# Kernel optimization log

Measured on AMD Instinct MI355X. Metric: run time of the kernel, lower is better.

The kernel has to match this reference:

```python
import jax, jax.numpy as jnp
import numpy as np

HEADS = 8
WH, WW = 8, 8
DIM = 256
B = 4096
N = WH * WW  # 64


def _rel_index():
    ch, cw = np.meshgrid(np.arange(WH), np.arange(WW), indexing='ij')
    coords = np.stack([ch.ravel(), cw.ravel()])  # (2, N)
    rel = coords[:, :, None] - coords[:, None, :]  # (2, N, N)
    rel = rel.transpose(1, 2, 0)
    rel[:, :, 0] += WH - 1
    rel[:, :, 1] += WW - 1
    rel[:, :, 0] *= 2 * WW - 1
    return jnp.asarray(rel.sum(-1), dtype=jnp.int32)  # (N, N)


def setup_inputs() -> dict:
    key = jax.random.key(0)
    ks = jax.random.split(key, 6)
    x = jax.random.normal(ks[0], (B, N, DIM), dtype=jnp.float32)
    attn_mask = jnp.zeros((1, HEADS, N, N), dtype=jnp.float32)
    w_qkv = jax.random.normal(ks[1], (3 * DIM, DIM), dtype=jnp.float32) * 0.02
    w_proj = jax.random.normal(ks[2], (DIM, DIM), dtype=jnp.float32) * 0.02
    b_proj = jax.random.normal(ks[3], (DIM,), dtype=jnp.float32) * 0.02
    table = jax.random.normal(ks[4], (225, HEADS), dtype=jnp.float32) * 0.02
    return {"x": x, "attn_mask": attn_mask, "w_qkv": w_qkv, "w_proj": w_proj,
            "b_proj": b_proj, "table": table, "rel_index": _rel_index()}


def reference(x, attn_mask, w_qkv, w_proj, b_proj, table, rel_index):
    Bn, Nn, C = x.shape
    hd = C // HEADS
    qkv = (x @ w_qkv.T).reshape(Bn, Nn, 3, HEADS, hd)
    q = qkv[:, :, 0].transpose(0, 2, 1, 3)  # (B,h,N,d)
    k = qkv[:, :, 1].transpose(0, 2, 1, 3)
    v = qkv[:, :, 2].transpose(0, 2, 1, 3)
    scale = 1.0 / jnp.sqrt(jnp.asarray(hd, dtype=x.dtype))
    attn = jnp.einsum('bhnd,bhmd->bhnm', q, k) * scale
    bias = table[rel_index]  # (N,N,h)
    attn = attn + bias.transpose(2, 0, 1)[None] + attn_mask
    attn = jax.nn.softmax(attn, axis=-1)
    out = jnp.einsum('bhnm,bhmd->bhnd', attn, v)
    out = out.transpose(0, 2, 1, 3).reshape(Bn, Nn, C)
    return out @ w_proj.T + b_proj
```

## Files before the change

kernel.cpp:

```cpp
#include <hip/hip_runtime.h>
#include <hip/hip_bf16.h>

#define HEADS 8
#define NTOK 64
#define DIM 256

typedef __attribute__((ext_vector_type(8))) short bf16x8;
typedef __attribute__((ext_vector_type(4))) short bf16x4;
typedef __attribute__((ext_vector_type(4))) float f32x4;
typedef unsigned short u16;

__device__ __forceinline__ u16 nf2bf(float f) {
    __hip_bfloat16 b = __float2bfloat16(f);
    return *reinterpret_cast<u16*>(&b);
}

__global__ void prep_kernel(const float* __restrict__ wqkv,
                            const float* __restrict__ wproj,
                            const float* __restrict__ table,
                            const int* __restrict__ rel_index,
                            const float* __restrict__ mask,
                            u16* __restrict__ wq_bf,
                            u16* __restrict__ wp_bf,
                            float* __restrict__ bias) {
    const int NQ = 768 * 256;
    const int NP = 256 * 256;
    const int NB = HEADS * NTOK * NTOK;
    int total = NQ + NP + NB;
    for (int i = blockIdx.x * blockDim.x + threadIdx.x; i < total;
         i += gridDim.x * blockDim.x) {
        if (i < NQ) {
            wq_bf[i] = nf2bf(wqkv[i]);
        } else if (i < NQ + NP) {
            wp_bf[i - NQ] = nf2bf(wproj[i - NQ]);
        } else {
            int j = i - (NQ + NP);
            int h = j >> 12;
            int nm = j & 4095;
            bias[j] = (table[rel_index[nm] * HEADS + h] + mask[j])
                      * 1.4426950408889634f;
        }
    }
}

__launch_bounds__(512, 2)
__global__ void win_attn_kernel(const float* __restrict__ x,
                                const u16* __restrict__ wq_bf,
                                const u16* __restrict__ wp_bf,
                                const float* __restrict__ bias,
                                const float* __restrict__ b_proj,
                                float* __restrict__ out) {
    __shared__ u16 smem[33792];
    u16* s_x = smem;
    u16* s_o = smem + 16896;

    const int b = blockIdx.x;
    const int tid = threadIdx.x;
    const int w = tid >> 6;
    const int l = tid & 63;
    const int l16 = l & 15;
    const int lhi = l >> 4;
    const int h = w;

    const u16* rq0 = wq_bf + (h * 32 + l16) * 256;
    const u16* rq1 = rq0 + 16 * 256;
    const u16* rk0 = wq_bf + (256 + h * 32 + l16) * 256;
    const u16* rk1 = rk0 + 16 * 256;
    const u16* rv0 = wq_bf + (512 + h * 32 + l16) * 256;
    const u16* rv1 = rv0 + 16 * 256;

    bf16x8 aq0 = *reinterpret_cast<const bf16x8*>(rq0 + lhi * 8);
    bf16x8 aq1 = *reinterpret_cast<const bf16x8*>(rq1 + lhi * 8);
    bf16x8 ak0 = *reinterpret_cast<const bf16x8*>(rk0 + lhi * 8);
    bf16x8 ak1 = *reinterpret_cast<const bf16x8*>(rk1 + lhi * 8);
    bf16x8 av0 = *reinterpret_cast<const bf16x8*>(rv0 + lhi * 8);
    bf16x8 av1 = *reinterpret_cast<const bf16x8*>(rv1 + lhi * 8);
    bf16x8 bq0 = *reinterpret_cast<const bf16x8*>(rq0 + 32 + lhi * 8);
    bf16x8 bq1 = *reinterpret_cast<const bf16x8*>(rq1 + 32 + lhi * 8);
    bf16x8 bk0 = *reinterpret_cast<const bf16x8*>(rk0 + 32 + lhi * 8);
    bf16x8 bk1 = *reinterpret_cast<const bf16x8*>(rk1 + 32 + lhi * 8);
    bf16x8 bv0 = *reinterpret_cast<const bf16x8*>(rv0 + 32 + lhi * 8);
    bf16x8 bv1 = *reinterpret_cast<const bf16x8*>(rv1 + 32 + lhi * 8);

    const float* xw = x + (size_t)b * (NTOK * DIM);
#pragma unroll
    for (int it = 0; it < 8; ++it) {
        int idx4 = tid + it * 512;
        float4 v = reinterpret_cast<const float4*>(xw)[idx4];
        int row = idx4 >> 6;
        int col = (idx4 & 63) * 4;
        ushort4 o;
        o.x = nf2bf(v.x); o.y = nf2bf(v.y); o.z = nf2bf(v.z); o.w = nf2bf(v.w);
        *reinterpret_cast<ushort4*>(&s_x[row * 264 + col]) = o;
    }
    __syncthreads();

    f32x4 qacc[2][4], kacc[2][4], vacc[4][2];
    const f32x4 zero = {0.f, 0.f, 0.f, 0.f};
#pragma unroll
    for (int ct = 0; ct < 2; ++ct)
#pragma unroll
        for (int tt = 0; tt < 4; ++tt) {
            qacc[ct][tt] = zero; kacc[ct][tt] = zero; vacc[tt][ct] = zero;
        }

    for (int ks = 0; ks < 8; ++ks) {
        const int k0 = ks * 32 + lhi * 8;
        bf16x8 xf[4];
#pragma unroll
        for (int tt = 0; tt < 4; ++tt)
            xf[tt] = *reinterpret_cast<const bf16x8*>(&s_x[(tt * 16 + l16) * 264 + k0]);
        bf16x8 nq0, nq1, nk0, nk1, nv0, nv1;
        if (ks < 6) {
            nq0 = *reinterpret_cast<const bf16x8*>(rq0 + k0 + 64);
            nq1 = *reinterpret_cast<const bf16x8*>(rq1 + k0 + 64);
            nk0 = *reinterpret_cast<const bf16x8*>(rk0 + k0 + 64);
            nk1 = *reinterpret_cast<const bf16x8*>(rk1 + k0 + 64);
            nv0 = *reinterpret_cast<const bf16x8*>(rv0 + k0 + 64);
            nv1 = *reinterpret_cast<const bf16x8*>(rv1 + k0 + 64);
        }
#pragma unroll
        for (int tt = 0; tt < 4; ++tt) {
            qacc[0][tt] = __builtin_amdgcn_mfma_f32_16x16x32_bf16(aq0, xf[tt], qacc[0][tt], 0, 0, 0);
            qacc[1][tt] = __builtin_amdgcn_mfma_f32_16x16x32_bf16(aq1, xf[tt], qacc[1][tt], 0, 0, 0);
            kacc[0][tt] = __builtin_amdgcn_mfma_f32_16x16x32_bf16(ak0, xf[tt], kacc[0][tt], 0, 0, 0);
            kacc[1][tt] = __builtin_amdgcn_mfma_f32_16x16x32_bf16(ak1, xf[tt], kacc[1][tt], 0, 0, 0);
            vacc[tt][0] = __builtin_amdgcn_mfma_f32_16x16x32_bf16(xf[tt], av0, vacc[tt][0], 0, 0, 0);
            vacc[tt][1] = __builtin_amdgcn_mfma_f32_16x16x32_bf16(xf[tt], av1, vacc[tt][1], 0, 0, 0);
        }
        aq0 = bq0; aq1 = bq1; ak0 = bk0; ak1 = bk1; av0 = bv0; av1 = bv1;
        bq0 = nq0; bq1 = nq1; bk0 = nk0; bk1 = nk1; bv0 = nv0; bv1 = nv1;
    }

    bf16x4 qf[4][2], kf[4][2], vf[4][2];
#pragma unroll
    for (int tt = 0; tt < 4; ++tt)
#pragma unroll
        for (int ct = 0; ct < 2; ++ct) {
            bf16x4 q, k, v;
#pragma unroll
            for (int r = 0; r < 4; ++r) {
                q[r] = (short)nf2bf(qacc[ct][tt][r]);
                k[r] = (short)nf2bf(kacc[ct][tt][r]);
                v[r] = (short)nf2bf(vacc[tt][ct][r]);
            }
            qf[tt][ct] = q; kf[tt][ct] = k; vf[tt][ct] = v;
        }

    {
        const float scale = 0.17677669529663687f * 1.4426950408889634f;
        const float* biash = bias + h * 4096;
        f32x4 bias_c[4], bias_n[4];
#pragma unroll
        for (int mt = 0; mt < 4; ++mt)
            bias_c[mt] = *reinterpret_cast<const f32x4*>(
                &biash[l16 * 64 + mt * 16 + lhi * 4]);

#pragma unroll
        for (int nt = 0; nt < 4; ++nt) {
            if (nt < 3) {
#pragma unroll
                for (int mt = 0; mt < 4; ++mt)
                    bias_n[mt] = *reinterpret_cast<const f32x4*>(
                        &biash[((nt + 1) * 16 + l16) * 64 + mt * 16 + lhi * 4]);
            }
            f32x4 sacc[4];
#pragma unroll
            for (int mt = 0; mt < 4; ++mt) {
                sacc[mt] = __builtin_amdgcn_mfma_f32_16x16x16bf16_1k(kf[mt][0], qf[nt][0], zero, 0, 0, 0);
                sacc[mt] = __builtin_amdgcn_mfma_f32_16x16x16bf16_1k(kf[mt][1], qf[nt][1], sacc[mt], 0, 0, 0);
            }
            float p[4][4];
            float sum = 0.f;
#pragma unroll
            for (int mt = 0; mt < 4; ++mt)
#pragma unroll
                for (int r = 0; r < 4; ++r) {
                    p[mt][r] = exp2f(sacc[mt][r] * scale + bias_c[mt][r]);
                    sum += p[mt][r];
                }
            sum += __shfl_xor(sum, 16, 64);
            sum += __shfl_xor(sum, 32, 64);
            float inv = 1.0f / sum;
            bf16x4 pf[4];
#pragma unroll
            for (int mt = 0; mt < 4; ++mt) {
                bf16x4 pk;
#pragma unroll
                for (int r = 0; r < 4; ++r) pk[r] = (short)nf2bf(p[mt][r]);
                pf[mt] = pk;
            }
            f32x4 oa0 = zero, oa1 = zero;
#pragma unroll
            for (int mt = 0; mt < 4; ++mt) {
                oa0 = __builtin_amdgcn_mfma_f32_16x16x16bf16_1k(vf[mt][0], pf[mt], oa0, 0, 0, 0);
                oa1 = __builtin_amdgcn_mfma_f32_16x16x16bf16_1k(vf[mt][1], pf[mt], oa1, 0, 0, 0);
            }
            {
                ushort4 o0, o1;
                o0.x = nf2bf(oa0[0] * inv); o0.y = nf2bf(oa0[1] * inv);
                o0.z = nf2bf(oa0[2] * inv); o0.w = nf2bf(oa0[3] * inv);
                o1.x = nf2bf(oa1[0] * inv); o1.y = nf2bf(oa1[1] * inv);
                o1.z = nf2bf(oa1[2] * inv); o1.w = nf2bf(oa1[3] * inv);
                u16* orow = &s_o[(nt * 16 + l16) * 264 + h * 32 + lhi * 4];
                *reinterpret_cast<ushort4*>(orow) = o0;
                *reinterpret_cast<ushort4*>(orow + 16) = o1;
            }
            if (nt < 3) {
#pragma unroll
                for (int mt = 0; mt < 4; ++mt) bias_c[mt] = bias_n[mt];
            }
        }
    }
    __syncthreads();

    f32x4 acc3[2][4];
#pragma unroll
    for (int t = 0; t < 2; ++t)
#pragma unroll
        for (int tt = 0; tt < 4; ++tt) acc3[t][tt] = zero;

    const u16* prow0 = wp_bf + (w * 16 + l16) * 256;
    const u16* prow1 = wp_bf + ((w + 8) * 16 + l16) * 256;
    bf16x8 wp0 = *reinterpret_cast<const bf16x8*>(prow0 + lhi * 8);
    bf16x8 wp1 = *reinterpret_cast<const bf16x8*>(prow1 + lhi * 8);
    for (int ks = 0; ks < 8; ++ks) {
        const int k0 = ks * 32 + lhi * 8;
        bf16x8 np0, np1;
        if (ks < 7) {
            np0 = *reinterpret_cast<const bf16x8*>(prow0 + k0 + 32);
            np1 = *reinterpret_cast<const bf16x8*>(prow1 + k0 + 32);
        }
#pragma unroll
        for (int tt = 0; tt < 4; ++tt) {
            bf16x8 of = *reinterpret_cast<const bf16x8*>(&s_o[(tt * 16 + l16) * 264 + k0]);
            acc3[0][tt] = __builtin_amdgcn_mfma_f32_16x16x32_bf16(wp0, of, acc3[0][tt], 0, 0, 0);
            acc3[1][tt] = __builtin_amdgcn_mfma_f32_16x16x32_bf16(wp1, of, acc3[1][tt], 0, 0, 0);
        }
        wp0 = np0; wp1 = np1;
    }
    float* outw = out + (size_t)b * (NTOK * DIM);
#pragma unroll
    for (int t = 0; t < 2; ++t) {
        int colb = (w + t * 8) * 16 + lhi * 4;
        float4 bp = *reinterpret_cast<const float4*>(&b_proj[colb]);
#pragma unroll
        for (int tt = 0; tt < 4; ++tt) {
            float4 o;
            o.x = acc3[t][tt][0] + bp.x;
            o.y = acc3[t][tt][1] + bp.y;
            o.z = acc3[t][tt][2] + bp.z;
            o.w = acc3[t][tt][3] + bp.w;
            *reinterpret_cast<float4*>(&outw[(tt * 16 + l16) * 256 + colb]) = o;
        }
    }
}

extern "C" void kernel_launch(void* const* d_in, const int* in_sizes, int n_in,
                              void* d_out, int out_size, void* d_ws, size_t ws_size,
                              hipStream_t stream) {
    const float* x     = (const float*)d_in[0];
    const float* mask  = (const float*)d_in[1];
    const float* wqkv  = (const float*)d_in[2];
    const float* wproj = (const float*)d_in[3];
    const float* bproj = (const float*)d_in[4];
    const float* table = (const float*)d_in[5];
    const int*   relix = (const int*)d_in[6];

    u16*   wq_bf = (u16*)d_ws;
    u16*   wp_bf = wq_bf + 768 * 256;
    float* bias  = (float*)(wp_bf + 256 * 256);

    prep_kernel<<<64, 512, 0, stream>>>(wqkv, wproj, table, relix, mask,
                                        wq_bf, wp_bf, bias);
    win_attn_kernel<<<4096, 512, 0, stream>>>(x, wq_bf, wp_bf, bias, bproj,
                                              (float*)d_out);
}
```

Measured before the change: 385.1 us.

## Process two windows per block and interleave QKV and projection GEMMs across them

Each block now handles two windows, halving the grid. The x load for the second window is issued before the first window's attention, and the second window's QKV GEMM is fused into one loop with the first window's output projection. The aim is to hide global-load latency and keep the MFMA units busy across stage boundaries. The cost is much higher register pressure from holding q/k/v fragments, accumulators and staged x together at launch bounds (512,2), which could cause spills. Weight loads in the fused loop also lose their software prefetch.

```diff
diff --git a/kernel.cpp b/kernel.cpp
--- a/kernel.cpp
+++ b/kernel.cpp
@@ -51,10 +51,12 @@
                                 const float* __restrict__ b_proj,
                                 float* __restrict__ out) {
     __shared__ u16 smem[33792];
-    u16* s_x = smem;
-    u16* s_o = smem + 16896;
-
-    const int b = blockIdx.x;
+    u16* buf0 = smem;
+    u16* buf1 = smem + 16896;
+
+    const int bid = blockIdx.x;
+    const int winA = bid * 2;
+    const int winB = bid * 2 + 1;
     const int tid = threadIdx.x;
     const int w = tid >> 6;
     const int l = tid & 63;
@@ -68,107 +70,116 @@
     const u16* rk1 = rk0 + 16 * 256;
     const u16* rv0 = wq_bf + (512 + h * 32 + l16) * 256;
     const u16* rv1 = rv0 + 16 * 256;
-
-    bf16x8 aq0 = *reinterpret_cast<const bf16x8*>(rq0 + lhi * 8);
-    bf16x8 aq1 = *reinterpret_cast<const bf16x8*>(rq1 + lhi * 8);
-    bf16x8 ak0 = *reinterpret_cast<const bf16x8*>(rk0 + lhi * 8);
-    bf16x8 ak1 = *reinterpret_cast<const bf16x8*>(rk1 + lhi * 8);
-    bf16x8 av0 = *reinterpret_cast<const bf16x8*>(rv0 + lhi * 8);
-    bf16x8 av1 = *reinterpret_cast<const bf16x8*>(rv1 + lhi * 8);
-    bf16x8 bq0 = *reinterpret_cast<const bf16x8*>(rq0 + 32 + lhi * 8);
-    bf16x8 bq1 = *reinterpret_cast<const bf16x8*>(rq1 + 32 + lhi * 8);
-    bf16x8 bk0 = *reinterpret_cast<const bf16x8*>(rk0 + 32 + lhi * 8);
-    bf16x8 bk1 = *reinterpret_cast<const bf16x8*>(rk1 + 32 + lhi * 8);
-    bf16x8 bv0 = *reinterpret_cast<const bf16x8*>(rv0 + 32 + lhi * 8);
-    bf16x8 bv1 = *reinterpret_cast<const bf16x8*>(rv1 + 32 + lhi * 8);
-
-    const float* xw = x + (size_t)b * (NTOK * DIM);
-#pragma unroll
-    for (int it = 0; it < 8; ++it) {
-        int idx4 = tid + it * 512;
-        float4 v = reinterpret_cast<const float4*>(xw)[idx4];
-        int row = idx4 >> 6;
-        int col = (idx4 & 63) * 4;
-        ushort4 o;
-        o.x = nf2bf(v.x); o.y = nf2bf(v.y); o.z = nf2bf(v.z); o.w = nf2bf(v.w);
-        *reinterpret_cast<ushort4*>(&s_x[row * 264 + col]) = o;
+    const u16* prow0 = wp_bf + (w * 16 + l16) * 256;
+    const u16* prow1 = wp_bf + ((w + 8) * 16 + l16) * 256;
+    const float* biash = bias + h * 4096;
+    const f32x4 zero = {0.f, 0.f, 0.f, 0.f};
+    const float scale = 0.17677669529663687f * 1.4426950408889634f;
+
+    const float4 bp0 = *reinterpret_cast<const float4*>(&b_proj[w * 16 + lhi * 4]);
+    const float4 bp1 = *reinterpret_cast<const float4*>(&b_proj[(w + 8) * 16 + lhi * 4]);
+
+    {
+        const float* xw = x + (size_t)winA * (NTOK * DIM);
+#pragma unroll
+        for (int it = 0; it < 8; ++it) {
+            int idx4 = tid + it * 512;
+            float4 v = reinterpret_cast<const float4*>(xw)[idx4];
+            int row = idx4 >> 6;
+            int col = (idx4 & 63) * 4;
+            ushort4 o;
+            o.x = nf2bf(v.x); o.y = nf2bf(v.y); o.z = nf2bf(v.z); o.w = nf2bf(v.w);
+            *reinterpret_cast<ushort4*>(&buf0[row * 264 + col]) = o;
+        }
     }
     __syncthreads();
 
-    f32x4 qacc[2][4], kacc[2][4], vacc[4][2];
-    const f32x4 zero = {0.f, 0.f, 0.f, 0.f};
-#pragma unroll
-    for (int ct = 0; ct < 2; ++ct)
-#pragma unroll
-        for (int tt = 0; tt < 4; ++tt) {
-            qacc[ct][tt] = zero; kacc[ct][tt] = zero; vacc[tt][ct] = zero;
-        }
-
-    for (int ks = 0; ks < 8; ++ks) {
-        const int k0 = ks * 32 + lhi * 8;
-        bf16x8 xf[4];
+    bf16x4 qfA[4][2], kfA[4][2], vfA[4][2];
+    {
+        f32x4 qacc[2][4], kacc[2][4], vacc[4][2];
+#pragma unroll
+        for (int ct = 0; ct < 2; ++ct)
+#pragma unroll
+            for (int tt = 0; tt < 4; ++tt) {
+                qacc[ct][tt] = zero; kacc[ct][tt] = zero; vacc[tt][ct] = zero;
+            }
+        bf16x8 aq0 = *reinterpret_cast<const bf16x8*>(rq0 + lhi * 8);
+        bf16x8 aq1 = *reinterpret_cast<const bf16x8*>(rq1 + lhi * 8);
+        bf16x8 ak0 = *reinterpret_cast<const bf16x8*>(rk0 + lhi * 8);
+        bf16x8 ak1 = *reinterpret_cast<const bf16x8*>(rk1 + lhi * 8);
+        bf16x8 av0 = *reinterpret_cast<const bf16x8*>(rv0 + lhi * 8);
+        bf16x8 av1 = *reinterpret_cast<const bf16x8*>(rv1 + lhi * 8);
+        bf16x8 bq0 = *reinterpret_cast<const bf16x8*>(rq0 + 32 + lhi * 8);
+        bf16x8 bq1 = *reinterpret_cast<const bf16x8*>(rq1 + 32 + lhi * 8);
+        bf16x8 bk0 = *reinterpret_cast<const bf16x8*>(rk0 + 32 + lhi * 8);
+        bf16x8 bk1 = *reinterpret_cast<const bf16x8*>(rk1 + 32 + lhi * 8);
+        bf16x8 bv0 = *reinterpret_cast<const bf16x8*>(rv0 + 32 + lhi * 8);
+        bf16x8 bv1 = *reinterpret_cast<const bf16x8*>(rv1 + 32 + lhi * 8);
+
+        for (int ks = 0; ks < 8; ++ks) {
+            const int k0 = ks * 32 + lhi * 8;
+            bf16x8 xf[4];
+#pragma unroll
+            for (int tt = 0; tt < 4; ++tt)
+                xf[tt] = *reinterpret_cast<const bf16x8*>(&buf0[(tt * 16 + l16) * 264 + k0]);
+            bf16x8 nq0, nq1, nk0, nk1, nv0, nv1;
+            if (ks < 6) {
+                nq0 = *reinterpret_cast<const bf16x8*>(rq0 + k0 + 64);
+                nq1 = *reinterpret_cast<const bf16x8*>(rq1 + k0 + 64);
+                nk0 = *reinterpret_cast<const bf16x8*>(rk0 + k0 + 64);
+                nk1 = *reinterpret_cast<const bf16x8*>(rk1 + k0 + 64);
+                nv0 = *reinterpret_cast<const bf16x8*>(rv0 + k0 + 64);
+                nv1 = *reinterpret_cast<const bf16x8*>(rv1 + k0 + 64);
+            }
+#pragma unroll
+            for (int tt = 0; tt < 4; ++tt) {
+                qacc[0][tt] = __builtin_amdgcn_mfma_f32_16x16x32_bf16(aq0, xf[tt], qacc[0][tt], 0, 0, 0);
+                qacc[1][tt] = __builtin_amdgcn_mfma_f32_16x16x32_bf16(aq1, xf[tt], qacc[1][tt], 0, 0, 0);
+                kacc[0][tt] = __builtin_amdgcn_mfma_f32_16x16x32_bf16(ak0, xf[tt], kacc[0][tt], 0, 0, 0);
+                kacc[1][tt] = __builtin_amdgcn_mfma_f32_16x16x32_bf16(ak1, xf[tt], kacc[1][tt], 0, 0, 0);
+                vacc[tt][0] = __builtin_amdgcn_mfma_f32_16x16x32_bf16(xf[tt], av0, vacc[tt][0], 0, 0, 0);
+                vacc[tt][1] = __builtin_amdgcn_mfma_f32_16x16x32_bf16(xf[tt], av1, vacc[tt][1], 0, 0, 0);
+            }
+            aq0 = bq0; aq1 = bq1; ak0 = bk0; ak1 = bk1; av0 = bv0; av1 = bv1;
+            bq0 = nq0; bq1 = nq1; bk0 = nk0; bk1 = nk1; bv0 = nv0; bv1 = nv1;
+        }
 #pragma unroll
         for (int tt = 0; tt < 4; ++tt)
-            xf[tt] = *reinterpret_cast<const bf16x8*>(&s_x[(tt * 16 + l16) * 264 + k0]);
-        bf16x8 nq0, nq1, nk0, nk1, nv0, nv1;
-        if (ks < 6) {
-            nq0 = *reinterpret_cast<const bf16x8*>(rq0 + k0 + 64);
-            nq1 = *reinterpret_cast<const bf16x8*>(rq1 + k0 + 64);
-            nk0 = *reinterpret_cast<const bf16x8*>(rk0 + k0 + 64);
-            nk1 = *reinterpret_cast<const bf16x8*>(rk1 + k0 + 64);
-            nv0 = *reinterpret_cast<const bf16x8*>(rv0 + k0 + 64);
-            nv1 = *reinterpret_cast<const bf16x8*>(rv1 + k0 + 64);
-        }
-#pragma unroll
-        for (int tt = 0; tt < 4; ++tt) {
-            qacc[0][tt] = __builtin_amdgcn_mfma_f32_16x16x32_bf16(aq0, xf[tt], qacc[0][tt], 0, 0, 0);
-            qacc[1][tt] = __builtin_amdgcn_mfma_f32_16x16x32_bf16(aq1, xf[tt], qacc[1][tt], 0, 0, 0);
-            kacc[0][tt] = __builtin_amdgcn_mfma_f32_16x16x32_bf16(ak0, xf[tt], kacc[0][tt], 0, 0, 0);
-            kacc[1][tt] = __builtin_amdgcn_mfma_f32_16x16x32_bf16(ak1, xf[tt], kacc[1][tt], 0, 0, 0);
-            vacc[tt][0] = __builtin_amdgcn_mfma_f32_16x16x32_bf16(xf[tt], av0, vacc[tt][0], 0, 0, 0);
-            vacc[tt][1] = __builtin_amdgcn_mfma_f32_16x16x32_bf16(xf[tt], av1, vacc[tt][1], 0, 0, 0);
-        }
-        aq0 = bq0; aq1 = bq1; ak0 = bk0; ak1 = bk1; av0 = bv0; av1 = bv1;
-        bq0 = nq0; bq1 = nq1; bk0 = nk0; bk1 = nk1; bv0 = nv0; bv1 = nv1;
-    }
-
-    bf16x4 qf[4][2], kf[4][2], vf[4][2];
-#pragma unroll
-    for (int tt = 0; tt < 4; ++tt)
-#pragma unroll
-        for (int ct = 0; ct < 2; ++ct) {
-            bf16x4 q, k, v;
-#pragma unroll
-            for (int r = 0; r < 4; ++r) {
-                q[r] = (short)nf2bf(qacc[ct][tt][r]);
-                k[r] = (short)nf2bf(kacc[ct][tt][r]);
-                v[r] = (short)nf2bf(vacc[tt][ct][r]);
-            }
-            qf[tt][ct] = q; kf[tt][ct] = k; vf[tt][ct] = v;
-        }
-
-    {
-        const float scale = 0.17677669529663687f * 1.4426950408889634f;
-        const float* biash = bias + h * 4096;
-        f32x4 bias_c[4], bias_n[4];
-#pragma unroll
-        for (int mt = 0; mt < 4; ++mt)
-            bias_c[mt] = *reinterpret_cast<const f32x4*>(
-                &biash[l16 * 64 + mt * 16 + lhi * 4]);
-
+#pragma unroll
+            for (int ct = 0; ct < 2; ++ct) {
+                bf16x4 q, k, v;
+#pragma unroll
+                for (int r = 0; r < 4; ++r) {
+                    q[r] = (short)nf2bf(qacc[ct][tt][r]);
+                    k[r] = (short)nf2bf(kacc[ct][tt][r]);
+                    v[r] = (short)nf2bf(vacc[tt][ct][r]);
+                }
+                qfA[tt][ct] = q; kfA[tt][ct] = k; vfA[tt][ct] = v;
+            }
+    }
+    __syncthreads();
+
+    float4 xs[8];
+    {
+        const float* xw = x + (size_t)winB * (NTOK * DIM);
+#pragma unroll
+        for (int it = 0; it < 8; ++it)
+            xs[it] = reinterpret_cast<const float4*>(xw)[tid + it * 512];
+    }
+
+    {
+        f32x4 bias_c[4];
 #pragma unroll
         for (int nt = 0; nt < 4; ++nt) {
-            if (nt < 3) {
-#pragma unroll
-                for (int mt = 0; mt < 4; ++mt)
-                    bias_n[mt] = *reinterpret_cast<const f32x4*>(
-                        &biash[((nt + 1) * 16 + l16) * 64 + mt * 16 + lhi * 4]);
-            }
+#pragma unroll
+            for (int mt = 0; mt < 4; ++mt)
+                bias_c[mt] = *reinterpret_cast<const f32x4*>(
+                    &biash[(nt * 16 + l16) * 64 + mt * 16 + lhi * 4]);
             f32x4 sacc[4];
 #pragma unroll
             for (int mt = 0; mt < 4; ++mt) {
-                sacc[mt] = __builtin_amdgcn_mfma_f32_16x16x16bf16_1k(kf[mt][0], qf[nt][0], zero, 0, 0, 0);
-                sacc[mt] = __builtin_amdgcn_mfma_f32_16x16x16bf16_1k(kf[mt][1], qf[nt][1], sacc[mt], 0, 0, 0);
+                sacc[mt] = __builtin_amdgcn_mfma_f32_16x16x16bf16_1k(kfA[mt][0], qfA[nt][0], zero, 0, 0, 0);
+                sacc[mt] = __builtin_amdgcn_mfma_f32_16x16x16bf16_1k(kfA[mt][1], qfA[nt][1], sacc[mt], 0, 0, 0);
             }
             float p[4][4];
             float sum = 0.f;
@@ -193,65 +204,184 @@
             f32x4 oa0 = zero, oa1 = zero;
 #pragma unroll
             for (int mt = 0; mt < 4; ++mt) {
-                oa0 = __builtin_amdgcn_mfma_f32_16x16x16bf16_1k(vf[mt][0], pf[mt], oa0, 0, 0, 0);
-                oa1 = __builtin_amdgcn_mfma_f32_16x16x16bf16_1k(vf[mt][1], pf[mt], oa1, 0, 0, 0);
-            }
-            {
-                ushort4 o0, o1;
-                o0.x = nf2bf(oa0[0] * inv); o0.y = nf2bf(oa0[1] * inv);
-                o0.z = nf2bf(oa0[2] * inv); o0.w = nf2bf(oa0[3] * inv);
-                o1.x = nf2bf(oa1[0] * inv); o1.y = nf2bf(oa1[1] * inv);
-                o1.z = nf2bf(oa1[2] * inv); o1.w = nf2bf(oa1[3] * inv);
-                u16* orow = &s_o[(nt * 16 + l16) * 264 + h * 32 + lhi * 4];
-                *reinterpret_cast<ushort4*>(orow) = o0;
-                *reinterpret_cast<ushort4*>(orow + 16) = o1;
-            }
-            if (nt < 3) {
-#pragma unroll
-                for (int mt = 0; mt < 4; ++mt) bias_c[mt] = bias_n[mt];
-            }
-        }
+                oa0 = __builtin_amdgcn_mfma_f32_16x16x16bf16_1k(vfA[mt][0], pf[mt], oa0, 0, 0, 0);
+                oa1 = __builtin_amdgcn_mfma_f32_16x16x16bf16_1k(vfA[mt][1], pf[mt], oa1, 0, 0, 0);
+            }
+            ushort4 o0, o1;
+            o0.x = nf2bf(oa0[0] * inv); o0.y = nf2bf(oa0[1] * inv);
+            o0.z = nf2bf(oa0[2] * inv); o0.w = nf2bf(oa0[3] * inv);
+            o1.x = nf2bf(oa1[0] * inv); o1.y = nf2bf(oa1[1] * inv);
+            o1.z = nf2bf(oa1[2] * inv); o1.w = nf2bf(oa1[3] * inv);
+            u16* orow = &buf0[(nt * 16 + l16) * 264 + h * 32 + lhi * 4];
+            *reinterpret_cast<ushort4*>(orow) = o0;
+            *reinterpret_cast<ushort4*>(orow + 16) = o1;
+        }
+    }
+
+#pragma unroll
+    for (int it = 0; it < 8; ++it) {
+        int idx4 = tid + it * 512;
+        int row = idx4 >> 6;
+        int col = (idx4 & 63) * 4;
+        ushort4 o;
+        o.x = nf2bf(xs[it].x); o.y = nf2bf(xs[it].y);
+        o.z = nf2bf(xs[it].z); o.w = nf2bf(xs[it].w);
+        *reinterpret_cast<ushort4*>(&buf1[row * 264 + col]) = o;
     }
     __syncthreads();
 
-    f32x4 acc3[2][4];
-#pragma unroll
-    for (int t = 0; t < 2; ++t)
-#pragma unroll
-        for (int tt = 0; tt < 4; ++tt) acc3[t][tt] = zero;
-
-    const u16* prow0 = wp_bf + (w * 16 + l16) * 256;
-    const u16* prow1 = wp_bf + ((w + 8) * 16 + l16) * 256;
-    bf16x8 wp0 = *reinterpret_cast<const bf16x8*>(prow0 + lhi * 8);
-    bf16x8 wp1 = *reinterpret_cast<const bf16x8*>(prow1 + lhi * 8);
-    for (int ks = 0; ks < 8; ++ks) {
-        const int k0 = ks * 32 + lhi * 8;
-        bf16x8 np0, np1;
-        if (ks < 7) {
-            np0 = *reinterpret_cast<const bf16x8*>(prow0 + k0 + 32);
-            np1 = *reinterpret_cast<const bf16x8*>(prow1 + k0 + 32);
-        }
-#pragma unroll
-        for (int tt = 0; tt < 4; ++tt) {
-            bf16x8 of = *reinterpret_cast<const bf16x8*>(&s_o[(tt * 16 + l16) * 264 + k0]);
-            acc3[0][tt] = __builtin_amdgcn_mfma_f32_16x16x32_bf16(wp0, of, acc3[0][tt], 0, 0, 0);
-            acc3[1][tt] = __builtin_amdgcn_mfma_f32_16x16x32_bf16(wp1, of, acc3[1][tt], 0, 0, 0);
-        }
-        wp0 = np0; wp1 = np1;
-    }
-    float* outw = out + (size_t)b * (NTOK * DIM);
-#pragma unroll
-    for (int t = 0; t < 2; ++t) {
-        int colb = (w + t * 8) * 16 + lhi * 4;
-        float4 bp = *reinterpret_cast<const float4*>(&b_proj[colb]);
+    bf16x4 qfB[4][2], kfB[4][2], vfB[4][2];
+    {
+        f32x4 acc3[2][4];
+        f32x4 qacc[2][4], kacc[2][4], vacc[4][2];
+#pragma unroll
+        for (int ct = 0; ct < 2; ++ct)
+#pragma unroll
+            for (int tt = 0; tt < 4; ++tt) {
+                acc3[ct][tt] = zero;
+                qacc[ct][tt] = zero; kacc[ct][tt] = zero; vacc[tt][ct] = zero;
+            }
+        for (int ks = 0; ks < 8; ++ks) {
+            const int k0 = ks * 32 + lhi * 8;
+            bf16x8 xf[4];
+#pragma unroll
+            for (int tt = 0; tt < 4; ++tt)
+                xf[tt] = *reinterpret_cast<const bf16x8*>(&buf1[(tt * 16 + l16) * 264 + k0]);
+            bf16x8 wq0 = *reinterpret_cast<const bf16x8*>(rq0 + k0);
+            bf16x8 wq1 = *reinterpret_cast<const bf16x8*>(rq1 + k0);
+            bf16x8 wk0 = *reinterpret_cast<const bf16x8*>(rk0 + k0);
+            bf16x8 wk1 = *reinterpret_cast<const bf16x8*>(rk1 + k0);
+            bf16x8 wv0 = *reinterpret_cast<const bf16x8*>(rv0 + k0);
+            bf16x8 wv1 = *reinterpret_cast<const bf16x8*>(rv1 + k0);
+            bf16x8 wp0 = *reinterpret_cast<const bf16x8*>(prow0 + k0);
+            bf16x8 wp1 = *reinterpret_cast<const bf16x8*>(prow1 + k0);
+#pragma unroll
+            for (int tt = 0; tt < 4; ++tt) {
+                bf16x8 of = *reinterpret_cast<const bf16x8*>(&buf0[(tt * 16 + l16) * 264 + k0]);
+                acc3[0][tt] = __builtin_amdgcn_mfma_f32_16x16x32_bf16(wp0, of, acc3[0][tt], 0, 0, 0);
+                acc3[1][tt] = __builtin_amdgcn_mfma_f32_16x16x32_bf16(wp1, of, acc3[1][tt], 0, 0, 0);
+                qacc[0][tt] = __builtin_amdgcn_mfma_f32_16x16x32_bf16(wq0, xf[tt], qacc[0][tt], 0, 0, 0);
+                qacc[1][tt] = __builtin_amdgcn_mfma_f32_16x16x32_bf16(wq1, xf[tt], qacc[1][tt], 0, 0, 0);
+                kacc[0][tt] = __builtin_amdgcn_mfma_f32_16x16x32_bf16(wk0, xf[tt], kacc[0][tt], 0, 0, 0);
+                kacc[1][tt] = __builtin_amdgcn_mfma_f32_16x16x32_bf16(wk1, xf[tt], kacc[1][tt], 0, 0, 0);
+                vacc[tt][0] = __builtin_amdgcn_mfma_f32_16x16x32_bf16(xf[tt], wv0, vacc[tt][0], 0, 0, 0);
+                vacc[tt][1] = __builtin_amdgcn_mfma_f32_16x16x32_bf16(xf[tt], wv1, vacc[tt][1], 0, 0, 0);
+            }
+        }
+        float* outw = out + (size_t)winA * (NTOK * DIM);
 #pragma unroll
         for (int tt = 0; tt < 4; ++tt) {
             float4 o;
-            o.x = acc3[t][tt][0] + bp.x;
-            o.y = acc3[t][tt][1] + bp.y;
-            o.z = acc3[t][tt][2] + bp.z;
-            o.w = acc3[t][tt][3] + bp.w;
-            *reinterpret_cast<float4*>(&outw[(tt * 16 + l16) * 256 + colb]) = o;
+            o.x = acc3[0][tt][0] + bp0.x; o.y = acc3[0][tt][1] + bp0.y;
+            o.z = acc3[0][tt][2] + bp0.z; o.w = acc3[0][tt][3] + bp0.w;
+            *reinterpret_cast<float4*>(&outw[(tt * 16 + l16) * 256 + w * 16 + lhi * 4]) = o;
+            float4 q;
+            q.x = acc3[1][tt][0] + bp1.x; q.y = acc3[1][tt][1] + bp1.y;
+            q.z = acc3[1][tt][2] + bp1.z; q.w = acc3[1][tt][3] + bp1.w;
+            *reinterpret_cast<float4*>(&outw[(tt * 16 + l16) * 256 + (w + 8) * 16 + lhi * 4]) = q;
+        }
+#pragma unroll
+        for (int tt = 0; tt < 4; ++tt)
+#pragma unroll
+            for (int ct = 0; ct < 2; ++ct) {
+                bf16x4 q, k, v;
+#pragma unroll
+                for (int r = 0; r < 4; ++r) {
+                    q[r] = (short)nf2bf(qacc[ct][tt][r]);
+                    k[r] = (short)nf2bf(kacc[ct][tt][r]);
+                    v[r] = (short)nf2bf(vacc[tt][ct][r]);
+                }
+                qfB[tt][ct] = q; kfB[tt][ct] = k; vfB[tt][ct] = v;
+            }
+    }
+    __syncthreads();
+
+    {
+        f32x4 bias_c[4];
+#pragma unroll
+        for (int nt = 0; nt < 4; ++nt) {
+#pragma unroll
+            for (int mt = 0; mt < 4; ++mt)
+                bias_c[mt] = *reinterpret_cast<const f32x4*>(
+                    &biash[(nt * 16 + l16) * 64 + mt * 16 + lhi * 4]);
+            f32x4 sacc[4];
+#pragma unroll
+            for (int mt = 0; mt < 4; ++mt) {
+                sacc[mt] = __builtin_amdgcn_mfma_f32_16x16x16bf16_1k(kfB[mt][0], qfB[nt][0], zero, 0, 0, 0);
+                sacc[mt] = __builtin_amdgcn_mfma_f32_16x16x16bf16_1k(kfB[mt][1], qfB[nt][1], sacc[mt], 0, 0, 0);
+            }
+            float p[4][4];
+            float sum = 0.f;
+#pragma unroll
+            for (int mt = 0; mt < 4; ++mt)
+#pragma unroll
+                for (int r = 0; r < 4; ++r) {
+                    p[mt][r] = exp2f(sacc[mt][r] * scale + bias_c[mt][r]);
+                    sum += p[mt][r];
+                }
+            sum += __shfl_xor(sum, 16, 64);
+            sum += __shfl_xor(sum, 32, 64);
+            float inv = 1.0f / sum;
+            bf16x4 pf[4];
+#pragma unroll
+            for (int mt = 0; mt < 4; ++mt) {
+                bf16x4 pk;
+#pragma unroll
+                for (int r = 0; r < 4; ++r) pk[r] = (short)nf2bf(p[mt][r]);
+                pf[mt] = pk;
+            }
+            f32x4 oa0 = zero, oa1 = zero;
+#pragma unroll
+            for (int mt = 0; mt < 4; ++mt) {
+                oa0 = __builtin_amdgcn_mfma_f32_16x16x16bf16_1k(vfB[mt][0], pf[mt], oa0, 0, 0, 0);
+                oa1 = __builtin_amdgcn_mfma_f32_16x16x16bf16_1k(vfB[mt][1], pf[mt], oa1, 0, 0, 0);
+            }
+            ushort4 o0, o1;
+            o0.x = nf2bf(oa0[0] * inv); o0.y = nf2bf(oa0[1] * inv);
+            o0.z = nf2bf(oa0[2] * inv); o0.w = nf2bf(oa0[3] * inv);
+            o1.x = nf2bf(oa1[0] * inv); o1.y = nf2bf(oa1[1] * inv);
+            o1.z = nf2bf(oa1[2] * inv); o1.w = nf2bf(oa1[3] * inv);
+            u16* orow = &buf1[(nt * 16 + l16) * 264 + h * 32 + lhi * 4];
+            *reinterpret_cast<ushort4*>(orow) = o0;
+            *reinterpret_cast<ushort4*>(orow + 16) = o1;
+        }
+    }
+    __syncthreads();
+
+    {
+        f32x4 acc3[2][4];
+#pragma unroll
+        for (int t = 0; t < 2; ++t)
+#pragma unroll
+            for (int tt = 0; tt < 4; ++tt) acc3[t][tt] = zero;
+        bf16x8 wp0 = *reinterpret_cast<const bf16x8*>(prow0 + lhi * 8);
+        bf16x8 wp1 = *reinterpret_cast<const bf16x8*>(prow1 + lhi * 8);
+        for (int ks = 0; ks < 8; ++ks) {
+            const int k0 = ks * 32 + lhi * 8;
+            bf16x8 np0, np1;
+            if (ks < 7) {
+                np0 = *reinterpret_cast<const bf16x8*>(prow0 + k0 + 32);
+                np1 = *reinterpret_cast<const bf16x8*>(prow1 + k0 + 32);
+            }
+#pragma unroll
+            for (int tt = 0; tt < 4; ++tt) {
+                bf16x8 of = *reinterpret_cast<const bf16x8*>(&buf1[(tt * 16 + l16) * 264 + k0]);
+                acc3[0][tt] = __builtin_amdgcn_mfma_f32_16x16x32_bf16(wp0, of, acc3[0][tt], 0, 0, 0);
+                acc3[1][tt] = __builtin_amdgcn_mfma_f32_16x16x32_bf16(wp1, of, acc3[1][tt], 0, 0, 0);
+            }
+            wp0 = np0; wp1 = np1;
+        }
+        float* outw = out + (size_t)winB * (NTOK * DIM);
+#pragma unroll
+        for (int tt = 0; tt < 4; ++tt) {
+            float4 o;
+            o.x = acc3[0][tt][0] + bp0.x; o.y = acc3[0][tt][1] + bp0.y;
+            o.z = acc3[0][tt][2] + bp0.z; o.w = acc3[0][tt][3] + bp0.w;
+            *reinterpret_cast<float4*>(&outw[(tt * 16 + l16) * 256 + w * 16 + lhi * 4]) = o;
+            float4 q;
+            q.x = acc3[1][tt][0] + bp1.x; q.y = acc3[1][tt][1] + bp1.y;
+            q.z = acc3[1][tt][2] + bp1.z; q.w = acc3[1][tt][3] + bp1.w;
+            *reinterpret_cast<float4*>(&outw[(tt * 16 + l16) * 256 + (w + 8) * 16 + lhi * 4]) = q;
         }
     }
 }
@@ -273,6 +403,6 @@
 
     prep_kernel<<<64, 512, 0, stream>>>(wqkv, wproj, table, relix, mask,
                                         wq_bf, wp_bf, bias);
-    win_attn_kernel<<<4096, 512, 0, stream>>>(x, wq_bf, wp_bf, bias, bproj,
+    win_attn_kernel<<<2048, 512, 0, stream>>>(x, wq_bf, wp_bf, bias, bproj,
                                               (float*)d_out);
 }
```

Result: slower. 422.5 us (+9.7%).

## Halve block size to four waves, each processing two heads sequentially

Applied to the files above, without the earlier changes.

Launches 256-thread blocks where each wave handles two attention heads in a loop and two output column pairs in the projection. The bias prefetch across query tiles is replaced by direct per-tile loads. This reduces threads per block and may ease register allocation, but with LDS fixed per block it halves resident waves per CU and serializes per-head work within a wave.

```diff
diff --git a/kernel.cpp b/kernel.cpp
--- a/kernel.cpp
+++ b/kernel.cpp
@@ -43,7 +43,7 @@
     }
 }
 
-__launch_bounds__(512, 2)
+__launch_bounds__(256, 2)
 __global__ void win_attn_kernel(const float* __restrict__ x,
                                 const u16* __restrict__ wq_bf,
                                 const u16* __restrict__ wp_bf,
@@ -60,32 +60,14 @@
     const int l = tid & 63;
     const int l16 = l & 15;
     const int lhi = l >> 4;
-    const int h = w;
-
-    const u16* rq0 = wq_bf + (h * 32 + l16) * 256;
-    const u16* rq1 = rq0 + 16 * 256;
-    const u16* rk0 = wq_bf + (256 + h * 32 + l16) * 256;
-    const u16* rk1 = rk0 + 16 * 256;
-    const u16* rv0 = wq_bf + (512 + h * 32 + l16) * 256;
-    const u16* rv1 = rv0 + 16 * 256;
-
-    bf16x8 aq0 = *reinterpret_cast<const bf16x8*>(rq0 + lhi * 8);
-    bf16x8 aq1 = *reinterpret_cast<const bf16x8*>(rq1 + lhi * 8);
-    bf16x8 ak0 = *reinterpret_cast<const bf16x8*>(rk0 + lhi * 8);
-    bf16x8 ak1 = *reinterpret_cast<const bf16x8*>(rk1 + lhi * 8);
-    bf16x8 av0 = *reinterpret_cast<const bf16x8*>(rv0 + lhi * 8);
-    bf16x8 av1 = *reinterpret_cast<const bf16x8*>(rv1 + lhi * 8);
-    bf16x8 bq0 = *reinterpret_cast<const bf16x8*>(rq0 + 32 + lhi * 8);
-    bf16x8 bq1 = *reinterpret_cast<const bf16x8*>(rq1 + 32 + lhi * 8);
-    bf16x8 bk0 = *reinterpret_cast<const bf16x8*>(rk0 + 32 + lhi * 8);
-    bf16x8 bk1 = *reinterpret_cast<const bf16x8*>(rk1 + 32 + lhi * 8);
-    bf16x8 bv0 = *reinterpret_cast<const bf16x8*>(rv0 + 32 + lhi * 8);
-    bf16x8 bv1 = *reinterpret_cast<const bf16x8*>(rv1 + 32 + lhi * 8);
+
+    const f32x4 zero = {0.f, 0.f, 0.f, 0.f};
+    const float scale = 0.17677669529663687f * 1.4426950408889634f;
 
     const float* xw = x + (size_t)b * (NTOK * DIM);
 #pragma unroll
-    for (int it = 0; it < 8; ++it) {
-        int idx4 = tid + it * 512;
+    for (int it = 0; it < 16; ++it) {
+        int idx4 = tid + it * 256;
         float4 v = reinterpret_cast<const float4*>(xw)[idx4];
         int row = idx4 >> 6;
         int col = (idx4 & 63) * 4;
@@ -95,75 +77,88 @@
     }
     __syncthreads();
 
-    f32x4 qacc[2][4], kacc[2][4], vacc[4][2];
-    const f32x4 zero = {0.f, 0.f, 0.f, 0.f};
-#pragma unroll
-    for (int ct = 0; ct < 2; ++ct)
-#pragma unroll
-        for (int tt = 0; tt < 4; ++tt) {
-            qacc[ct][tt] = zero; kacc[ct][tt] = zero; vacc[tt][ct] = zero;
-        }
-
-    for (int ks = 0; ks < 8; ++ks) {
-        const int k0 = ks * 32 + lhi * 8;
-        bf16x8 xf[4];
+#pragma unroll 1
+    for (int hh = 0; hh < 2; ++hh) {
+        const int h = w + hh * 4;
+
+        const u16* rq0 = wq_bf + (h * 32 + l16) * 256;
+        const u16* rq1 = rq0 + 16 * 256;
+        const u16* rk0 = wq_bf + (256 + h * 32 + l16) * 256;
+        const u16* rk1 = rk0 + 16 * 256;
+        const u16* rv0 = wq_bf + (512 + h * 32 + l16) * 256;
+        const u16* rv1 = rv0 + 16 * 256;
+
+        f32x4 qacc[2][4], kacc[2][4], vacc[4][2];
+#pragma unroll
+        for (int ct = 0; ct < 2; ++ct)
+#pragma unroll
+            for (int tt = 0; tt < 4; ++tt) {
+                qacc[ct][tt] = zero; kacc[ct][tt] = zero; vacc[tt][ct] = zero;
+            }
+        bf16x8 aq0 = *reinterpret_cast<const bf16x8*>(rq0 + lhi * 8);
+        bf16x8 aq1 = *reinterpret_cast<const bf16x8*>(rq1 + lhi * 8);
+        bf16x8 ak0 = *reinterpret_cast<const bf16x8*>(rk0 + lhi * 8);
+        bf16x8 ak1 = *reinterpret_cast<const bf16x8*>(rk1 + lhi * 8);
+        bf16x8 av0 = *reinterpret_cast<const bf16x8*>(rv0 + lhi * 8);
+        bf16x8 av1 = *reinterpret_cast<const bf16x8*>(rv1 + lhi * 8);
+        bf16x8 bq0 = *reinterpret_cast<const bf16x8*>(rq0 + 32 + lhi * 8);
+        bf16x8 bq1 = *reinterpret_cast<const bf16x8*>(rq1 + 32 + lhi * 8);
+        bf16x8 bk0 = *reinterpret_cast<const bf16x8*>(rk0 + 32 + lhi * 8);
+        bf16x8 bk1 = *reinterpret_cast<const bf16x8*>(rk1 + 32 + lhi * 8);
+        bf16x8 bv0 = *reinterpret_cast<const bf16x8*>(rv0 + 32 + lhi * 8);
+        bf16x8 bv1 = *reinterpret_cast<const bf16x8*>(rv1 + 32 + lhi * 8);
+
+        for (int ks = 0; ks < 8; ++ks) {
+            const int k0 = ks * 32 + lhi * 8;
+            bf16x8 xf[4];
+#pragma unroll
+            for (int tt = 0; tt < 4; ++tt)
+                xf[tt] = *reinterpret_cast<const bf16x8*>(&s_x[(tt * 16 + l16) * 264 + k0]);
+            bf16x8 nq0, nq1, nk0, nk1, nv0, nv1;
+            if (ks < 6) {
+                nq0 = *reinterpret_cast<const bf16x8*>(rq0 + k0 + 64);
+                nq1 = *reinterpret_cast<const bf16x8*>(rq1 + k0 + 64);
+                nk0 = *reinterpret_cast<const bf16x8*>(rk0 + k0 + 64);
+                nk1 = *reinterpret_cast<const bf16x8*>(rk1 + k0 + 64);
+                nv0 = *reinterpret_cast<const bf16x8*>(rv0 + k0 + 64);
+                nv1 = *reinterpret_cast<const bf16x8*>(rv1 + k0 + 64);
+            }
+#pragma unroll
+            for (int tt = 0; tt < 4; ++tt) {
+                qacc[0][tt] = __builtin_amdgcn_mfma_f32_16x16x32_bf16(aq0, xf[tt], qacc[0][tt], 0, 0, 0);
+                qacc[1][tt] = __builtin_amdgcn_mfma_f32_16x16x32_bf16(aq1, xf[tt], qacc[1][tt], 0, 0, 0);
+                kacc[0][tt] = __builtin_amdgcn_mfma_f32_16x16x32_bf16(ak0, xf[tt], kacc[0][tt], 0, 0, 0);
+                kacc[1][tt] = __builtin_amdgcn_mfma_f32_16x16x32_bf16(ak1, xf[tt], kacc[1][tt], 0, 0, 0);
+                vacc[tt][0] = __builtin_amdgcn_mfma_f32_16x16x32_bf16(xf[tt], av0, vacc[tt][0], 0, 0, 0);
+                vacc[tt][1] = __builtin_amdgcn_mfma_f32_16x16x32_bf16(xf[tt], av1, vacc[tt][1], 0, 0, 0);
+            }
+            aq0 = bq0; aq1 = bq1; ak0 = bk0; ak1 = bk1; av0 = bv0; av1 = bv1;
+            bq0 = nq0; bq1 = nq1; bk0 = nk0; bk1 = nk1; bv0 = nv0; bv1 = nv1;
+        }
+
+        bf16x4 qf[4][2], kf[4][2], vf[4][2];
 #pragma unroll
         for (int tt = 0; tt < 4; ++tt)
-            xf[tt] = *reinterpret_cast<const bf16x8*>(&s_x[(tt * 16 + l16) * 264 + k0]);
-        bf16x8 nq0, nq1, nk0, nk1, nv0, nv1;
-        if (ks < 6) {
-            nq0 = *reinterpret_cast<const bf16x8*>(rq0 + k0 + 64);
-            nq1 = *reinterpret_cast<const bf16x8*>(rq1 + k0 + 64);
-            nk0 = *reinterpret_cast<const bf16x8*>(rk0 + k0 + 64);
-            nk1 = *reinterpret_cast<const bf16x8*>(rk1 + k0 + 64);
-            nv0 = *reinterpret_cast<const bf16x8*>(rv0 + k0 + 64);
-            nv1 = *reinterpret_cast<const bf16x8*>(rv1 + k0 + 64);
-        }
-#pragma unroll
-        for (int tt = 0; tt < 4; ++tt) {
-            qacc[0][tt] = __builtin_amdgcn_mfma_f32_16x16x32_bf16(aq0, xf[tt], qacc[0][tt], 0, 0, 0);
-            qacc[1][tt] = __builtin_amdgcn_mfma_f32_16x16x32_bf16(aq1, xf[tt], qacc[1][tt], 0, 0, 0);
-            kacc[0][tt] = __builtin_amdgcn_mfma_f32_16x16x32_bf16(ak0, xf[tt], kacc[0][tt], 0, 0, 0);
-            kacc[1][tt] = __builtin_amdgcn_mfma_f32_16x16x32_bf16(ak1, xf[tt], kacc[1][tt], 0, 0, 0);
-            vacc[tt][0] = __builtin_amdgcn_mfma_f32_16x16x32_bf16(xf[tt], av0, vacc[tt][0], 0, 0, 0);
-            vacc[tt][1] = __builtin_amdgcn_mfma_f32_16x16x32_bf16(xf[tt], av1, vacc[tt][1], 0, 0, 0);
-        }
-        aq0 = bq0; aq1 = bq1; ak0 = bk0; ak1 = bk1; av0 = bv0; av1 = bv1;
-        bq0 = nq0; bq1 = nq1; bk0 = nk0; bk1 = nk1; bv0 = nv0; bv1 = nv1;
-    }
-
-    bf16x4 qf[4][2], kf[4][2], vf[4][2];
-#pragma unroll
-    for (int tt = 0; tt < 4; ++tt)
-#pragma unroll
-        for (int ct = 0; ct < 2; ++ct) {
-            bf16x4 q, k, v;
-#pragma unroll
-            for (int r = 0; r < 4; ++r) {
-                q[r] = (short)nf2bf(qacc[ct][tt][r]);
-                k[r] = (short)nf2bf(kacc[ct][tt][r]);
-                v[r] = (short)nf2bf(vacc[tt][ct][r]);
-            }
-            qf[tt][ct] = q; kf[tt][ct] = k; vf[tt][ct] = v;
-        }
-
-    {
-        const float scale = 0.17677669529663687f * 1.4426950408889634f;
+#pragma unroll
+            for (int ct = 0; ct < 2; ++ct) {
+                bf16x4 q, k, v;
+#pragma unroll
+                for (int r = 0; r < 4; ++r) {
+                    q[r] = (short)nf2bf(qacc[ct][tt][r]);
+                    k[r] = (short)nf2bf(kacc[ct][tt][r]);
+                    v[r] = (short)nf2bf(vacc[tt][ct][r]);
+                }
+                qf[tt][ct] = q; kf[tt][ct] = k; vf[tt][ct] = v;
+            }
+
         const float* biash = bias + h * 4096;
-        f32x4 bias_c[4], bias_n[4];
-#pragma unroll
-        for (int mt = 0; mt < 4; ++mt)
-            bias_c[mt] = *reinterpret_cast<const f32x4*>(
-                &biash[l16 * 64 + mt * 16 + lhi * 4]);
-
 #pragma unroll
         for (int nt = 0; nt < 4; ++nt) {
-            if (nt < 3) {
-#pragma unroll
-                for (int mt = 0; mt < 4; ++mt)
-                    bias_n[mt] = *reinterpret_cast<const f32x4*>(
-                        &biash[((nt + 1) * 16 + l16) * 64 + mt * 16 + lhi * 4]);
-            }
+            f32x4 bias_c[4];
+#pragma unroll
+            for (int mt = 0; mt < 4; ++mt)
+                bias_c[mt] = *reinterpret_cast<const f32x4*>(
+                    &biash[(nt * 16 + l16) * 64 + mt * 16 + lhi * 4]);
             f32x4 sacc[4];
 #pragma unroll
             for (int mt = 0; mt < 4; ++mt) {
@@ -196,62 +191,59 @@
                 oa0 = __builtin_amdgcn_mfma_f32_16x16x16bf16_1k(vf[mt][0], pf[mt], oa0, 0, 0, 0);
                 oa1 = __builtin_amdgcn_mfma_f32_16x16x16bf16_1k(vf[mt][1], pf[mt], oa1, 0, 0, 0);
             }
-            {
-                ushort4 o0, o1;
-                o0.x = nf2bf(oa0[0] * inv); o0.y = nf2bf(oa0[1] * inv);
-                o0.z = nf2bf(oa0[2] * inv); o0.w = nf2bf(oa0[3] * inv);
-                o1.x = nf2bf(oa1[0] * inv); o1.y = nf2bf(oa1[1] * inv);
-                o1.z = nf2bf(oa1[2] * inv); o1.w = nf2bf(oa1[3] * inv);
-                u16* orow = &s_o[(nt * 16 + l16) * 264 + h * 32 + lhi * 4];
-                *reinterpret_cast<ushort4*>(orow) = o0;
-                *reinterpret_cast<ushort4*>(orow + 16) = o1;
-            }
-            if (nt < 3) {
-#pragma unroll
-                for (int mt = 0; mt < 4; ++mt) bias_c[mt] = bias_n[mt];
-            }
+            ushort4 o0, o1;
+            o0.x = nf2bf(oa0[0] * inv); o0.y = nf2bf(oa0[1] * inv);
+            o0.z = nf2bf(oa0[2] * inv); o0.w = nf2bf(oa0[3] * inv);
+            o1.x = nf2bf(oa1[0] * inv); o1.y = nf2bf(oa1[1] * inv);
+            o1.z = nf2bf(oa1[2] * inv); o1.w = nf2bf(oa1[3] * inv);
+            u16* orow = &s_o[(nt * 16 + l16) * 264 + h * 32 + lhi * 4];
+            *reinterpret_cast<ushort4*>(orow) = o0;
+            *reinterpret_cast<ushort4*>(orow + 16) = o1;
         }
     }
     __syncthreads();
 
-    f32x4 acc3[2][4];
-#pragma unroll
-    for (int t = 0; t < 2; ++t)
-#pragma unroll
-        for (int tt = 0; tt < 4; ++tt) acc3[t][tt] = zero;
-
-    const u16* prow0 = wp_bf + (w * 16 + l16) * 256;
-    const u16* prow1 = wp_bf + ((w + 8) * 16 + l16) * 256;
-    bf16x8 wp0 = *reinterpret_cast<const bf16x8*>(prow0 + lhi * 8);
-    bf16x8 wp1 = *reinterpret_cast<const bf16x8*>(prow1 + lhi * 8);
-    for (int ks = 0; ks < 8; ++ks) {
-        const int k0 = ks * 32 + lhi * 8;
-        bf16x8 np0, np1;
-        if (ks < 7) {
-            np0 = *reinterpret_cast<const bf16x8*>(prow0 + k0 + 32);
-            np1 = *reinterpret_cast<const bf16x8*>(prow1 + k0 + 32);
-        }
-#pragma unroll
-        for (int tt = 0; tt < 4; ++tt) {
-            bf16x8 of = *reinterpret_cast<const bf16x8*>(&s_o[(tt * 16 + l16) * 264 + k0]);
-            acc3[0][tt] = __builtin_amdgcn_mfma_f32_16x16x32_bf16(wp0, of, acc3[0][tt], 0, 0, 0);
-            acc3[1][tt] = __builtin_amdgcn_mfma_f32_16x16x32_bf16(wp1, of, acc3[1][tt], 0, 0, 0);
-        }
-        wp0 = np0; wp1 = np1;
-    }
     float* outw = out + (size_t)b * (NTOK * DIM);
-#pragma unroll
-    for (int t = 0; t < 2; ++t) {
-        int colb = (w + t * 8) * 16 + lhi * 4;
-        float4 bp = *reinterpret_cast<const float4*>(&b_proj[colb]);
+#pragma unroll 1
+    for (int pp = 0; pp < 2; ++pp) {
+        const int c0 = w + pp * 8;
+        const u16* prow0 = wp_bf + (c0 * 16 + l16) * 256;
+        const u16* prow1 = wp_bf + ((c0 + 4) * 16 + l16) * 256;
+        f32x4 acc3[2][4];
+#pragma unroll
+        for (int t = 0; t < 2; ++t)
+#pragma unroll
+            for (int tt = 0; tt < 4; ++tt) acc3[t][tt] = zero;
+
+        bf16x8 wp0 = *reinterpret_cast<const bf16x8*>(prow0 + lhi * 8);
+        bf16x8 wp1 = *reinterpret_cast<const bf16x8*>(prow1 + lhi * 8);
+        for (int ks = 0; ks < 8; ++ks) {
+            const int k0 = ks * 32 + lhi * 8;
+            bf16x8 np0, np1;
+            if (ks < 7) {
+                np0 = *reinterpret_cast<const bf16x8*>(prow0 + k0 + 32);
+                np1 = *reinterpret_cast<const bf16x8*>(prow1 + k0 + 32);
+            }
+#pragma unroll
+            for (int tt = 0; tt < 4; ++tt) {
+                bf16x8 of = *reinterpret_cast<const bf16x8*>(&s_o[(tt * 16 + l16) * 264 + k0]);
+                acc3[0][tt] = __builtin_amdgcn_mfma_f32_16x16x32_bf16(wp0, of, acc3[0][tt], 0, 0, 0);
+                acc3[1][tt] = __builtin_amdgcn_mfma_f32_16x16x32_bf16(wp1, of, acc3[1][tt], 0, 0, 0);
+            }
+            wp0 = np0; wp1 = np1;
+        }
+        const float4 bpa = *reinterpret_cast<const float4*>(&b_proj[c0 * 16 + lhi * 4]);
+        const float4 bpb = *reinterpret_cast<const float4*>(&b_proj[(c0 + 4) * 16 + lhi * 4]);
 #pragma unroll
         for (int tt = 0; tt < 4; ++tt) {
             float4 o;
-            o.x = acc3[t][tt][0] + bp.x;
-            o.y = acc3[t][tt][1] + bp.y;
-            o.z = acc3[t][tt][2] + bp.z;
-            o.w = acc3[t][tt][3] + bp.w;
-            *reinterpret_cast<float4*>(&outw[(tt * 16 + l16) * 256 + colb]) = o;
+            o.x = acc3[0][tt][0] + bpa.x; o.y = acc3[0][tt][1] + bpa.y;
+            o.z = acc3[0][tt][2] + bpa.z; o.w = acc3[0][tt][3] + bpa.w;
+            *reinterpret_cast<float4*>(&outw[(tt * 16 + l16) * 256 + c0 * 16 + lhi * 4]) = o;
+            float4 q;
+            q.x = acc3[1][tt][0] + bpb.x; q.y = acc3[1][tt][1] + bpb.y;
+            q.z = acc3[1][tt][2] + bpb.z; q.w = acc3[1][tt][3] + bpb.w;
+            *reinterpret_cast<float4*>(&outw[(tt * 16 + l16) * 256 + (c0 + 4) * 16 + lhi * 4]) = q;
         }
     }
 }
@@ -273,6 +265,6 @@
 
     prep_kernel<<<64, 512, 0, stream>>>(wqkv, wproj, table, relix, mask,
                                         wq_bf, wp_bf, bias);
-    win_attn_kernel<<<4096, 512, 0, stream>>>(x, wq_bf, wp_bf, bias, bproj,
+    win_attn_kernel<<<4096, 256, 0, stream>>>(x, wq_bf, wp_bf, bias, bproj,
                                               (float*)d_out);
 }
```

After: 476.1 us. 23.6% more time.
